# Optimization experiments

Measured on AMD Instinct MI355X. Metric: run time of the kernel, lower is better.

## Reference

```python
import jax, jax.numpy as jnp
import numpy as np
import math

B, S, D, H, FF = 4, 1024, 1024, 16, 4096
DK = D // H
EPS = 1e-6


def _gelu(x):
    return 0.5 * x * (1 + jnp.tanh(math.sqrt(2 / math.pi) * (x + 0.044715 * x ** 3)))


def _layernorm(x, g, b):
    # torch LayerNorm clone: unbiased std, divide by (std + eps)
    mean = jnp.mean(x, axis=-1, keepdims=True)
    var = jnp.sum((x - mean) ** 2, axis=-1, keepdims=True) / (x.shape[-1] - 1)
    std = jnp.sqrt(var)
    return g * (x - mean) / (std + EPS) + b


def setup_inputs() -> dict:
    key = jax.random.key(0)
    ks = jax.random.split(key, 16)
    sc_d = 1.0 / math.sqrt(D)
    sc_ff = 1.0 / math.sqrt(FF)
    inp = {
        "query": jax.random.normal(ks[0], (B, S, D), jnp.float32),
        "key": jax.random.normal(ks[1], (B, S, D), jnp.float32),
        "value": jax.random.normal(ks[2], (B, S, D), jnp.float32),
        "mask": jnp.ones((B, S), jnp.int32),
        "Wq": jax.random.normal(ks[3], (D, D), jnp.float32) * sc_d,
        "bq": jnp.zeros((D,), jnp.float32),
        "Wk": jax.random.normal(ks[4], (D, D), jnp.float32) * sc_d,
        "bk": jnp.zeros((D,), jnp.float32),
        "Wv": jax.random.normal(ks[5], (D, D), jnp.float32) * sc_d,
        "bv": jnp.zeros((D,), jnp.float32),
        "Wo": jax.random.normal(ks[6], (D, D), jnp.float32) * sc_d,
        "bo": jnp.zeros((D,), jnp.float32),
        "W1": jax.random.normal(ks[7], (FF, D), jnp.float32) * sc_d,
        "b1": jnp.zeros((FF,), jnp.float32),
        "W2": jax.random.normal(ks[8], (D, FF), jnp.float32) * sc_ff,
        "b2": jnp.zeros((D,), jnp.float32),
        "g1": jnp.ones((D,), jnp.float32),
        "be1": jnp.zeros((D,), jnp.float32),
        "g2": jnp.ones((D,), jnp.float32),
        "be2": jnp.zeros((D,), jnp.float32),
    }
    return inp


def reference(query, key, value, mask, Wq, bq, Wk, bk, Wv, bv, Wo, bo,
              W1, b1, W2, b2, g1, be1, g2, be2):
    # self-attention: q = k = v = query (with_external=False)
    def proj(x, W, b):
        return (x @ W.T + b).reshape(B, S, H, DK).transpose(0, 2, 1, 3)  # [B,H,S,DK]

    q = proj(query, Wq, bq)
    k = proj(query, Wk, bk)
    v = proj(query, Wv, bv)
    scores = jnp.einsum("bhqd,bhkd->bhqk", q, k) / math.sqrt(DK)
    # 2D mask [B,S] broadcasts as [B,1,1,S] over key positions
    scores = jnp.where(mask[:, None, None, :] == 0, -1e9, scores)
    p = jax.nn.softmax(scores, axis=-1)
    attn = jnp.einsum("bhqk,bhkd->bhqd", p, v)
    attn = attn.transpose(0, 2, 1, 3).reshape(B, S, D)
    x = attn @ Wo.T + bo
    x = _layernorm(query + x, g1, be1)
    residual = x
    h1 = x @ W1.T + b1
    x2 = _gelu(h1 @ W2.T + b2)  # note: gelu applied AFTER fc2, per source
    return _layernorm(residual + x2, g2, be2)
```

## Files before the change

### kernel.cpp

```cpp
#include <hip/hip_runtime.h>
#include <hip/hip_bf16.h>
#include <math.h>

typedef __bf16 bf16;
typedef __bf16 bf16x8 __attribute__((ext_vector_type(8)));
typedef float floatx4 __attribute__((ext_vector_type(4)));

#define NT 4096
#define DMODEL 1024
#define NHEAD 16
#define DHEAD 64
#define FFDIM 4096

__device__ __forceinline__ void load_lds16(const void* g, void* l) {
    __builtin_amdgcn_global_load_lds(
        (const __attribute__((address_space(1))) void*)g,
        (__attribute__((address_space(3))) void*)l,
        16, 0, 0);
}

__device__ __forceinline__ unsigned short f2bf(float f) {
    bf16 h = (bf16)f;
    return __builtin_bit_cast(unsigned short, h);
}

__device__ __forceinline__ float gelu_f(float v) {
    return 0.5f * v * (1.0f + tanhf(0.7978845608028654f * (v + 0.044715f * v * v * v)));
}

__global__ __launch_bounds__(256) void cast_kernel(
    const float* __restrict__ q, const float* __restrict__ wq, const float* __restrict__ wk,
    const float* __restrict__ wv, const float* __restrict__ wo, const float* __restrict__ w1,
    const float* __restrict__ w2, const float* __restrict__ bq, const float* __restrict__ bk,
    const float* __restrict__ bv, bf16* __restrict__ xbf, bf16* __restrict__ wqkv,
    bf16* __restrict__ wob, bf16* __restrict__ w1b, bf16* __restrict__ w2b,
    float* __restrict__ bqkv)
{
    int gid = blockIdx.x * 256 + threadIdx.x;
    if (gid < 3072)
        bqkv[gid] = gid < 1024 ? bq[gid] : (gid < 2048 ? bk[gid - 1024] : bv[gid - 2048]);

    const float4* src;
    ushort4* dst;
    int off = gid;
    if (off < 1048576)                  { src = (const float4*)q;  dst = (ushort4*)xbf; }
    else if ((off -= 1048576) < 262144) { src = (const float4*)wq; dst = (ushort4*)wqkv; }
    else if ((off -= 262144) < 262144)  { src = (const float4*)wk; dst = (ushort4*)wqkv + 262144; }
    else if ((off -= 262144) < 262144)  { src = (const float4*)wv; dst = (ushort4*)wqkv + 524288; }
    else if ((off -= 262144) < 262144)  { src = (const float4*)wo; dst = (ushort4*)wob; }
    else if ((off -= 262144) < 1048576) { src = (const float4*)w1; dst = (ushort4*)w1b; }
    else { off -= 1048576;                src = (const float4*)w2; dst = (ushort4*)w2b; }

    float4 v = src[off];
    ushort4 u;
    u.x = f2bf(v.x); u.y = f2bf(v.y); u.z = f2bf(v.z); u.w = f2bf(v.w);
    dst[off] = u;
}

template <int EPI, int TN>
__global__ __launch_bounds__(256) void gemm_bt(
    const bf16* __restrict__ A, const bf16* __restrict__ Wt,
    const float* __restrict__ bias, const float* __restrict__ res,
    void* __restrict__ outp, int M, int N, int K)
{
    constexpr int NJ = TN / 32;
    __shared__ __align__(16) bf16 As[128 * 64];
    __shared__ __align__(16) bf16 Bs[TN * 64];

    const int t = threadIdx.x;
    const int lane = t & 63, wave = t >> 6;
    const int l15 = lane & 15, quad = lane >> 4;
    const int wm = wave & 1, wn = wave >> 1;
    const int m0 = blockIdx.x * 128, n0 = blockIdx.y * TN;

    floatx4 acc[4][NJ] = {};

    auto issue_loads = [&](int k0) {
        #pragma unroll
        for (int i = 0; i < 4; ++i) {
            int l = t + i * 256;
            int row = l >> 3, ch = (l & 7) ^ (row & 7);
            load_lds16(A + (size_t)(m0 + row) * K + k0 + ch * 8,
                       &As[(size_t)(i * 256 + wave * 64) * 8]);
        }
        #pragma unroll
        for (int i = 0; i < TN / 32; ++i) {
            int l = t + i * 256;
            int row = l >> 3, ch = (l & 7) ^ (row & 7);
            load_lds16(Wt + (size_t)(n0 + row) * K + k0 + ch * 8,
                       &Bs[(size_t)(i * 256 + wave * 64) * 8]);
        }
    };

    const int nk = K >> 6;
    issue_loads(0);

    for (int it = 0; it < nk; ++it) {
        __syncthreads();

        bf16x8 af[2][4], bfr[2][NJ];
        #pragma unroll
        for (int ks = 0; ks < 2; ++ks) {
            #pragma unroll
            for (int i = 0; i < 4; ++i) {
                int row = wm * 64 + i * 16 + l15;
                int pc = (ks * 4 + quad) ^ (row & 7);
                af[ks][i] = *(const bf16x8*)&As[row * 64 + pc * 8];
            }
            #pragma unroll
            for (int j = 0; j < NJ; ++j) {
                int row = wn * (TN / 2) + j * 16 + l15;
                int pc = (ks * 4 + quad) ^ (row & 7);
                bfr[ks][j] = *(const bf16x8*)&Bs[row * 64 + pc * 8];
            }
        }

        __syncthreads();

        if (it + 1 < nk) issue_loads((it + 1) << 6);

        #pragma unroll
        for (int ks = 0; ks < 2; ++ks)
            #pragma unroll
            for (int i = 0; i < 4; ++i)
                #pragma unroll
                for (int j = 0; j < NJ; ++j)
                    acc[i][j] = __builtin_amdgcn_mfma_f32_16x16x32_bf16(af[ks][i], bfr[ks][j], acc[i][j], 0, 0, 0);
    }

    const int mbase = m0 + wm * 64, nbase = n0 + wn * (TN / 2);
    #pragma unroll
    for (int i = 0; i < 4; ++i) {
        #pragma unroll
        for (int j = 0; j < NJ; ++j) {
            int col = nbase + j * 16 + l15;
            float bv = bias[col];
            #pragma unroll
            for (int r = 0; r < 4; ++r) {
                int row = mbase + i * 16 + quad * 4 + r;
                size_t idx = (size_t)row * N + col;
                float v = acc[i][j][r] + bv;
                if (EPI == 0) {
                    ((bf16*)outp)[idx] = (bf16)v;
                } else if (EPI == 1) {
                    ((float*)outp)[idx] = v + res[idx];
                } else {
                    ((float*)outp)[idx] = res[idx] + gelu_f(v);
                }
            }
        }
    }
}

__global__ __launch_bounds__(256) void transpose_v(const bf16* __restrict__ qkv,
                                                   bf16* __restrict__ vt)
{
    __shared__ bf16 tile[64 * 65];
    const int t = threadIdx.x;
    const int bh = blockIdx.y, bb = bh >> 4, h = bh & 15;
    const int s0 = blockIdx.x * 64;

    #pragma unroll
    for (int i = 0; i < 2; ++i) {
        int l = t + i * 256;
        int sl = l >> 3, c = (l & 7) * 8;
        bf16x8 v = *(const bf16x8*)(qkv + (size_t)(bb * 1024 + s0 + sl) * 3072 + 2048 + h * 64 + c);
        #pragma unroll
        for (int j = 0; j < 8; ++j) tile[sl * 65 + c + j] = v[j];
    }
    __syncthreads();
    #pragma unroll
    for (int i = 0; i < 2; ++i) {
        int l = t + i * 256;
        int dl = l >> 3, sc = (l & 7) * 8;
        bf16x8 v;
        #pragma unroll
        for (int j = 0; j < 8; ++j) v[j] = tile[(sc + j) * 65 + dl];
        *(bf16x8*)(vt + (size_t)(bh * 64 + dl) * 1024 + s0 + sc) = v;
    }
}

__global__ __launch_bounds__(256, 4) void flash_attn(
    const bf16* __restrict__ QKV, const bf16* __restrict__ VT,
    const int* __restrict__ mask, bf16* __restrict__ outp)
{
    __shared__ __align__(16) bf16 QPs[64 * 64];
    __shared__ __align__(16) bf16 Ks[2][64 * 64];
    __shared__ __align__(16) bf16 VTs[2][64 * 64];

    const int t = threadIdx.x;
    const int lane = t & 63, wave = t >> 6;
    const int l15 = lane & 15, quad = lane >> 4;
    const int bh = blockIdx.x, bb = bh >> 4, h = bh & 15;
    const int q0 = blockIdx.y * 64;

    #pragma unroll
    for (int i = 0; i < 2; ++i) {
        int l = t + i * 256;
        int row = l >> 3, c = (l & 7) ^ (row & 7);
        load_lds16(QKV + (size_t)(bb * 1024 + q0 + row) * 3072 + h * 64 + c * 8,
                   &QPs[(size_t)(i * 256 + wave * 64) * 8]);
    }

    auto stage_kv = [&](int buf, int kt) {
        #pragma unroll
        for (int i = 0; i < 2; ++i) {
            int l = t + i * 256;
            int row = l >> 3, c = (l & 7) ^ (row & 7);
            load_lds16(QKV + (size_t)(bb * 1024 + kt + row) * 3072 + 1024 + h * 64 + c * 8,
                       &Ks[buf][(size_t)(i * 256 + wave * 64) * 8]);
            load_lds16(VT + (size_t)(bh * 64 + row) * 1024 + kt + c * 8,
                       &VTs[buf][(size_t)(i * 256 + wave * 64) * 8]);
        }
    };
    stage_kv(0, 0);

    floatx4 acc_o[4] = {};
    float m_st[4], l_st[4];
    #pragma unroll
    for (int r = 0; r < 4; ++r) { m_st[r] = -1e30f; l_st[r] = 0.f; }

    __syncthreads();

    bf16x8 aq[2];
    #pragma unroll
    for (int ks = 0; ks < 2; ++ks) {
        int row = wave * 16 + l15;
        int pc = (ks * 4 + quad) ^ (row & 7);
        aq[ks] = *(const bf16x8*)&QPs[row * 64 + pc * 8];
    }

    const float SC2 = 0.18033688011112042f;
    const float MB  = -1.442695e9f;
    const int* mrow = mask + bb * 1024 + l15;

    for (int kt = 0; kt < 1024; kt += 64) {
        const int buf = (kt >> 6) & 1;
        __syncthreads();
        if (kt + 64 < 1024) stage_kv(buf ^ 1, kt + 64);

        float mb[4];
        #pragma unroll
        for (int nt = 0; nt < 4; ++nt)
            mb[nt] = mrow[kt + nt * 16] ? 0.f : MB;

        bf16x8 kf[2][4], vf[2][4];
        #pragma unroll
        for (int ks = 0; ks < 2; ++ks)
            #pragma unroll
            for (int nt = 0; nt < 4; ++nt) {
                int row = nt * 16 + l15;
                int pc = (ks * 4 + quad) ^ (row & 7);
                kf[ks][nt] = *(const bf16x8*)&Ks[buf][row * 64 + pc * 8];
                vf[ks][nt] = *(const bf16x8*)&VTs[buf][row * 64 + pc * 8];
            }

        floatx4 s[4] = {};
        #pragma unroll
        for (int ks = 0; ks < 2; ++ks)
            #pragma unroll
            for (int nt = 0; nt < 4; ++nt)
                s[nt] = __builtin_amdgcn_mfma_f32_16x16x32_bf16(aq[ks], kf[ks][nt], s[nt], 0, 0, 0);

        float sv[4][4];
        #pragma unroll
        for (int nt = 0; nt < 4; ++nt)
            #pragma unroll
            for (int r = 0; r < 4; ++r)
                sv[nt][r] = fmaf(s[nt][r], SC2, mb[nt]);

        float pmax[4];
        bool need = false;
        #pragma unroll
        for (int r = 0; r < 4; ++r) {
            float mx = fmaxf(fmaxf(sv[0][r], sv[1][r]), fmaxf(sv[2][r], sv[3][r]));
            #pragma unroll
            for (int d = 8; d >= 1; d >>= 1) mx = fmaxf(mx, __shfl_xor(mx, d, 64));
            pmax[r] = mx;
            need |= (mx > m_st[r] + 12.0f);
        }

        if (__any(need)) {
            #pragma unroll
            for (int r = 0; r < 4; ++r) {
                float mnew = fmaxf(m_st[r], pmax[r]);
                float al = __builtin_amdgcn_exp2f(m_st[r] - mnew);
                m_st[r] = mnew;
                l_st[r] *= al;
                #pragma unroll
                for (int nt = 0; nt < 4; ++nt) acc_o[nt][r] *= al;
            }
        }

        #pragma unroll
        for (int r = 0; r < 4; ++r) {
            int rowL = wave * 16 + quad * 4 + r;
            float rs = 0.f;
            #pragma unroll
            for (int nt = 0; nt < 4; ++nt) {
                float p = __builtin_amdgcn_exp2f(sv[nt][r] - m_st[r]);
                rs += p;
                int col = nt * 16 + l15;
                int pc = (col >> 3) ^ (rowL & 7);
                QPs[rowL * 64 + pc * 8 + (col & 7)] = (bf16)p;
            }
            l_st[r] += rs;
        }

        #pragma unroll
        for (int ks = 0; ks < 2; ++ks) {
            int row = wave * 16 + l15;
            int pc = (ks * 4 + quad) ^ (row & 7);
            bf16x8 ap = *(const bf16x8*)&QPs[row * 64 + pc * 8];
            #pragma unroll
            for (int nt = 0; nt < 4; ++nt)
                acc_o[nt] = __builtin_amdgcn_mfma_f32_16x16x32_bf16(ap, vf[ks][nt], acc_o[nt], 0, 0, 0);
        }
    }

    float linv[4];
    #pragma unroll
    for (int r = 0; r < 4; ++r) {
        float l = l_st[r];
        #pragma unroll
        for (int d = 8; d >= 1; d >>= 1) l += __shfl_xor(l, d, 64);
        linv[r] = __builtin_amdgcn_rcpf(l);
    }
    #pragma unroll
    for (int nt = 0; nt < 4; ++nt)
        #pragma unroll
        for (int r = 0; r < 4; ++r) {
            int qrow = q0 + wave * 16 + quad * 4 + r;
            int dd = nt * 16 + l15;
            outp[(size_t)(bb * 1024 + qrow) * 1024 + h * 64 + dd] = (bf16)(acc_o[nt][r] * linv[r]);
        }
}

__global__ __launch_bounds__(256) void layernorm_k(
    const float* __restrict__ x, const float* __restrict__ g, const float* __restrict__ b,
    bf16* __restrict__ obf, float* __restrict__ of)
{
    const int row = blockIdx.x;
    float4 v = ((const float4*)(x + (size_t)row * 1024))[threadIdx.x];
    float s = v.x + v.y + v.z + v.w;
    float s2 = v.x * v.x + v.y * v.y + v.z * v.z + v.w * v.w;
    #pragma unroll
    for (int o = 32; o >= 1; o >>= 1) {
        s += __shfl_down(s, o, 64);
        s2 += __shfl_down(s2, o, 64);
    }
    __shared__ float red[8];
    if ((threadIdx.x & 63) == 0) {
        red[threadIdx.x >> 6] = s;
        red[4 + (threadIdx.x >> 6)] = s2;
    }
    __syncthreads();
    s = red[0] + red[1] + red[2] + red[3];
    s2 = red[4] + red[5] + red[6] + red[7];
    float mean = s * (1.f / 1024.f);
    float var = fmaxf(0.f, s2 - 1024.f * mean * mean) * (1.f / 1023.f);
    float inv = 1.f / (sqrtf(var) + 1e-6f);
    float4 gg = ((const float4*)g)[threadIdx.x];
    float4 bb = ((const float4*)b)[threadIdx.x];
    float4 o;
    o.x = gg.x * (v.x - mean) * inv + bb.x;
    o.y = gg.y * (v.y - mean) * inv + bb.y;
    o.z = gg.z * (v.z - mean) * inv + bb.z;
    o.w = gg.w * (v.w - mean) * inv + bb.w;
    if (of) ((float4*)(of + (size_t)row * 1024))[threadIdx.x] = o;
    if (obf) {
        ushort4 u;
        u.x = f2bf(o.x); u.y = f2bf(o.y); u.z = f2bf(o.z); u.w = f2bf(o.w);
        ((ushort4*)(obf + (size_t)row * 1024))[threadIdx.x] = u;
    }
}

constexpr size_t OFF_XBF   = 0;
constexpr size_t OFF_WQKV  = OFF_XBF + 8388608;
constexpr size_t OFF_BQKV  = OFF_WQKV + 6291456;
constexpr size_t OFF_WO    = OFF_BQKV + 16384;
constexpr size_t OFF_W1    = OFF_WO + 2097152;
constexpr size_t OFF_W2    = OFF_W1 + 8388608;
constexpr size_t OFF_QKV   = OFF_W2 + 8388608;
constexpr size_t OFF_VT    = OFF_QKV + 25165824;
constexpr size_t OFF_XRES1 = OFF_VT + 8388608;
constexpr size_t OFF_X1BF  = OFF_XRES1 + 16777216;
constexpr size_t OFF_X1F   = OFF_X1BF + 8388608;
constexpr size_t OFF_H1    = OFF_X1F + 16777216;

extern "C" void kernel_launch(void* const* d_in, const int* in_sizes, int n_in,
                              void* d_out, int out_size, void* d_ws, size_t ws_size,
                              hipStream_t stream)
{
    const float* query = (const float*)d_in[0];
    const int*   maskp = (const int*)d_in[3];
    const float* Wq = (const float*)d_in[4];
    const float* bq = (const float*)d_in[5];
    const float* Wk = (const float*)d_in[6];
    const float* bk = (const float*)d_in[7];
    const float* Wv = (const float*)d_in[8];
    const float* bv = (const float*)d_in[9];
    const float* Wo = (const float*)d_in[10];
    const float* bo = (const float*)d_in[11];
    const float* W1 = (const float*)d_in[12];
    const float* b1 = (const float*)d_in[13];
    const float* W2 = (const float*)d_in[14];
    const float* b2 = (const float*)d_in[15];
    const float* g1 = (const float*)d_in[16];
    const float* be1 = (const float*)d_in[17];
    const float* g2 = (const float*)d_in[18];
    const float* be2 = (const float*)d_in[19];

    char* ws = (char*)d_ws;
    bf16*  xbf   = (bf16*)(ws + OFF_XBF);
    bf16*  wqkv  = (bf16*)(ws + OFF_WQKV);
    float* bqkv  = (float*)(ws + OFF_BQKV);
    bf16*  wob   = (bf16*)(ws + OFF_WO);
    bf16*  w1b   = (bf16*)(ws + OFF_W1);
    bf16*  w2b   = (bf16*)(ws + OFF_W2);
    bf16*  qkv   = (bf16*)(ws + OFF_QKV);
    bf16*  vt    = (bf16*)(ws + OFF_VT);
    float* xres1 = (float*)(ws + OFF_XRES1);
    bf16*  x1bf  = (bf16*)(ws + OFF_X1BF);
    float* x1f   = (float*)(ws + OFF_X1F);
    bf16*  h1    = (bf16*)(ws + OFF_H1);
    bf16*  attn  = (bf16*)(ws + OFF_XBF);
    float* xres2 = (float*)(ws + OFF_QKV);
    float* outf  = (float*)d_out;

    cast_kernel<<<16384, 256, 0, stream>>>(query, Wq, Wk, Wv, Wo, W1, W2, bq, bk, bv,
                                           xbf, wqkv, wob, w1b, w2b, bqkv);
    gemm_bt<0, 128><<<dim3(32, 24), 256, 0, stream>>>(xbf, wqkv, bqkv, nullptr, qkv, NT, 3072, 1024);
    transpose_v<<<dim3(16, 64), 256, 0, stream>>>(qkv, vt);
    flash_attn<<<dim3(64, 16), 256, 0, stream>>>(qkv, vt, maskp, attn);
    gemm_bt<1, 64><<<dim3(32, 16), 256, 0, stream>>>(attn, wob, bo, query, xres1, NT, 1024, 1024);
    layernorm_k<<<4096, 256, 0, stream>>>(xres1, g1, be1, x1bf, x1f);
    gemm_bt<0, 128><<<dim3(32, 32), 256, 0, stream>>>(x1bf, w1b, b1, nullptr, h1, NT, 4096, 1024);
    gemm_bt<2, 64><<<dim3(32, 16), 256, 0, stream>>>(h1, w2b, b2, x1f, xres2, NT, 1024, 4096);
    layernorm_k<<<4096, 256, 0, stream>>>(xres2, g2, be2, nullptr, outf);
}
```

Measured before the change: 353.0 us.

## Compute transposed scores in flash attention to keep P in registers

Swaps the MFMA operand order so each lane holds a query row's scores, permuting the K row staging so the P fragment lands directly in the A-operand layout for the PV MFMA. This removes the LDS round-trip for P and the separate QPs buffer; Q is staged through a spare V buffer. Row max and sum now need only two cross-lane shuffles, and a wave-uniform fast path skips per-element mask handling when all keys are valid. The cost is extra shuffles to broadcast rescale factors and the final normalizers, and a correctness dependency on the permuted key-row mapping.

```diff
diff --git a/kernel.cpp b/kernel.cpp
--- a/kernel.cpp
+++ b/kernel.cpp
@@ -184,7 +184,6 @@
     const bf16* __restrict__ QKV, const bf16* __restrict__ VT,
     const int* __restrict__ mask, bf16* __restrict__ outp)
 {
-    __shared__ __align__(16) bf16 QPs[64 * 64];
     __shared__ __align__(16) bf16 Ks[2][64 * 64];
     __shared__ __align__(16) bf16 VTs[2][64 * 64];
 
@@ -199,15 +198,26 @@
         int l = t + i * 256;
         int row = l >> 3, c = (l & 7) ^ (row & 7);
         load_lds16(QKV + (size_t)(bb * 1024 + q0 + row) * 3072 + h * 64 + c * 8,
-                   &QPs[(size_t)(i * 256 + wave * 64) * 8]);
-    }
+                   &VTs[1][(size_t)(i * 256 + wave * 64) * 8]);
+    }
+    __syncthreads();
+
+    bf16x8 aq[2];
+    #pragma unroll
+    for (int ks = 0; ks < 2; ++ks) {
+        int row = wave * 16 + l15;
+        int pc = (ks * 4 + quad) ^ (row & 7);
+        aq[ks] = *(const bf16x8*)&VTs[1][row * 64 + pc * 8];
+    }
+    __syncthreads();
 
     auto stage_kv = [&](int buf, int kt) {
         #pragma unroll
         for (int i = 0; i < 2; ++i) {
             int l = t + i * 256;
             int row = l >> 3, c = (l & 7) ^ (row & 7);
-            load_lds16(QKV + (size_t)(bb * 1024 + kt + row) * 3072 + 1024 + h * 64 + c * 8,
+            int gr = (row & 32) | ((row & 12) << 1) | ((row & 16) >> 2) | (row & 3);
+            load_lds16(QKV + (size_t)(bb * 1024 + kt + gr) * 3072 + 1024 + h * 64 + c * 8,
                        &Ks[buf][(size_t)(i * 256 + wave * 64) * 8]);
             load_lds16(VT + (size_t)(bh * 64 + row) * 1024 + kt + c * 8,
                        &VTs[buf][(size_t)(i * 256 + wave * 64) * 8]);
@@ -216,35 +226,19 @@
     stage_kv(0, 0);
 
     floatx4 acc_o[4] = {};
-    float m_st[4], l_st[4];
-    #pragma unroll
-    for (int r = 0; r < 4; ++r) { m_st[r] = -1e30f; l_st[r] = 0.f; }
-
-    __syncthreads();
-
-    bf16x8 aq[2];
-    #pragma unroll
-    for (int ks = 0; ks < 2; ++ks) {
-        int row = wave * 16 + l15;
-        int pc = (ks * 4 + quad) ^ (row & 7);
-        aq[ks] = *(const bf16x8*)&QPs[row * 64 + pc * 8];
-    }
-
+    float m_st = -1e30f, l_st = 0.f;
     const float SC2 = 0.18033688011112042f;
     const float MB  = -1.442695e9f;
-    const int* mrow = mask + bb * 1024 + l15;
+    const int* mrow = mask + bb * 1024;
 
     for (int kt = 0; kt < 1024; kt += 64) {
         const int buf = (kt >> 6) & 1;
         __syncthreads();
         if (kt + 64 < 1024) stage_kv(buf ^ 1, kt + 64);
 
-        float mb[4];
-        #pragma unroll
-        for (int nt = 0; nt < 4; ++nt)
-            mb[nt] = mrow[kt + nt * 16] ? 0.f : MB;
-
-        bf16x8 kf[2][4], vf[2][4];
+        int mv = mrow[kt + lane];
+
+        bf16x8 kf[2][4];
         #pragma unroll
         for (int ks = 0; ks < 2; ++ks)
             #pragma unroll
@@ -252,7 +246,6 @@
                 int row = nt * 16 + l15;
                 int pc = (ks * 4 + quad) ^ (row & 7);
                 kf[ks][nt] = *(const bf16x8*)&Ks[buf][row * 64 + pc * 8];
-                vf[ks][nt] = *(const bf16x8*)&VTs[buf][row * 64 + pc * 8];
             }
 
         floatx4 s[4] = {};
@@ -260,80 +253,91 @@
         for (int ks = 0; ks < 2; ++ks)
             #pragma unroll
             for (int nt = 0; nt < 4; ++nt)
-                s[nt] = __builtin_amdgcn_mfma_f32_16x16x32_bf16(aq[ks], kf[ks][nt], s[nt], 0, 0, 0);
+                s[nt] = __builtin_amdgcn_mfma_f32_16x16x32_bf16(kf[ks][nt], aq[ks], s[nt], 0, 0, 0);
+
+        bf16x8 vf[2][4];
+        #pragma unroll
+        for (int ks = 0; ks < 2; ++ks)
+            #pragma unroll
+            for (int nt2 = 0; nt2 < 4; ++nt2) {
+                int row = nt2 * 16 + l15;
+                int pc = (ks * 4 + quad) ^ (row & 7);
+                vf[ks][nt2] = *(const bf16x8*)&VTs[buf][row * 64 + pc * 8];
+            }
 
         float sv[4][4];
+        if (__all(mv != 0)) {
+            #pragma unroll
+            for (int nt = 0; nt < 4; ++nt)
+                #pragma unroll
+                for (int r = 0; r < 4; ++r)
+                    sv[nt][r] = s[nt][r] * SC2;
+        } else {
+            #pragma unroll
+            for (int nt = 0; nt < 4; ++nt)
+                #pragma unroll
+                for (int r = 0; r < 4; ++r) {
+                    int kg = ((nt >> 1) << 5) | (quad << 3) | ((nt & 1) << 2) | r;
+                    int mk = __shfl(mv, kg, 64);
+                    sv[nt][r] = fmaf(s[nt][r], SC2, mk ? 0.f : MB);
+                }
+        }
+
+        float mx = sv[0][0];
         #pragma unroll
         for (int nt = 0; nt < 4; ++nt)
             #pragma unroll
             for (int r = 0; r < 4; ++r)
-                sv[nt][r] = fmaf(s[nt][r], SC2, mb[nt]);
-
-        float pmax[4];
-        bool need = false;
-        #pragma unroll
-        for (int r = 0; r < 4; ++r) {
-            float mx = fmaxf(fmaxf(sv[0][r], sv[1][r]), fmaxf(sv[2][r], sv[3][r]));
-            #pragma unroll
-            for (int d = 8; d >= 1; d >>= 1) mx = fmaxf(mx, __shfl_xor(mx, d, 64));
-            pmax[r] = mx;
-            need |= (mx > m_st[r] + 12.0f);
-        }
-
-        if (__any(need)) {
+                mx = fmaxf(mx, sv[nt][r]);
+        mx = fmaxf(mx, __shfl_xor(mx, 16, 64));
+        mx = fmaxf(mx, __shfl_xor(mx, 32, 64));
+
+        if (__any(mx > m_st + 12.0f)) {
+            float mnew = fmaxf(m_st, mx);
+            float al = __builtin_amdgcn_exp2f(m_st - mnew);
+            m_st = mnew;
+            l_st *= al;
             #pragma unroll
             for (int r = 0; r < 4; ++r) {
-                float mnew = fmaxf(m_st[r], pmax[r]);
-                float al = __builtin_amdgcn_exp2f(m_st[r] - mnew);
-                m_st[r] = mnew;
-                l_st[r] *= al;
+                float alr = __shfl(al, quad * 4 + r, 64);
                 #pragma unroll
-                for (int nt = 0; nt < 4; ++nt) acc_o[nt][r] *= al;
-            }
-        }
-
-        #pragma unroll
-        for (int r = 0; r < 4; ++r) {
-            int rowL = wave * 16 + quad * 4 + r;
-            float rs = 0.f;
-            #pragma unroll
-            for (int nt = 0; nt < 4; ++nt) {
-                float p = __builtin_amdgcn_exp2f(sv[nt][r] - m_st[r]);
+                for (int nt2 = 0; nt2 < 4; ++nt2) acc_o[nt2][r] *= alr;
+            }
+        }
+
+        bf16x8 pa[2];
+        float rs = 0.f;
+        #pragma unroll
+        for (int nt = 0; nt < 4; ++nt)
+            #pragma unroll
+            for (int r = 0; r < 4; ++r) {
+                float p = __builtin_amdgcn_exp2f(sv[nt][r] - m_st);
                 rs += p;
-                int col = nt * 16 + l15;
-                int pc = (col >> 3) ^ (rowL & 7);
-                QPs[rowL * 64 + pc * 8 + (col & 7)] = (bf16)p;
-            }
-            l_st[r] += rs;
-        }
-
-        #pragma unroll
-        for (int ks = 0; ks < 2; ++ks) {
-            int row = wave * 16 + l15;
-            int pc = (ks * 4 + quad) ^ (row & 7);
-            bf16x8 ap = *(const bf16x8*)&QPs[row * 64 + pc * 8];
-            #pragma unroll
-            for (int nt = 0; nt < 4; ++nt)
-                acc_o[nt] = __builtin_amdgcn_mfma_f32_16x16x32_bf16(ap, vf[ks][nt], acc_o[nt], 0, 0, 0);
-        }
-    }
-
-    float linv[4];
+                pa[nt >> 1][(nt & 1) * 4 + r] = (bf16)p;
+            }
+        l_st += rs;
+
+        #pragma unroll
+        for (int ks = 0; ks < 2; ++ks)
+            #pragma unroll
+            for (int nt2 = 0; nt2 < 4; ++nt2)
+                acc_o[nt2] = __builtin_amdgcn_mfma_f32_16x16x32_bf16(pa[ks], vf[ks][nt2], acc_o[nt2], 0, 0, 0);
+    }
+
+    float lt = l_st;
+    lt += __shfl_xor(lt, 16, 64);
+    lt += __shfl_xor(lt, 32, 64);
     #pragma unroll
     for (int r = 0; r < 4; ++r) {
-        float l = l_st[r];
-        #pragma unroll
-        for (int d = 8; d >= 1; d >>= 1) l += __shfl_xor(l, d, 64);
-        linv[r] = __builtin_amdgcn_rcpf(l);
-    }
-    #pragma unroll
-    for (int nt = 0; nt < 4; ++nt)
-        #pragma unroll
-        for (int r = 0; r < 4; ++r) {
-            int qrow = q0 + wave * 16 + quad * 4 + r;
-            int dd = nt * 16 + l15;
-            outp[(size_t)(bb * 1024 + qrow) * 1024 + h * 64 + dd] = (bf16)(acc_o[nt][r] * linv[r]);
-        }
+        float lr = __shfl(lt, quad * 4 + r, 64);
+        float linv = __builtin_amdgcn_rcpf(lr);
+        int qrow = q0 + wave * 16 + quad * 4 + r;
+        #pragma unroll
+        for (int nt2 = 0; nt2 < 4; ++nt2) {
+            int dd = nt2 * 16 + l15;
+            outp[(size_t)(bb * 1024 + qrow) * 1024 + h * 64 + dd] = (bf16)(acc_o[nt2][r] * linv);
+        }
+    }
 }
 
 __global__ __launch_bounds__(256) void layernorm_k(
```

Result: faster. 344.0 us (-2.5%).
